# Kernel tuning notes

Hardware: AMD Instinct MI355X
Metric: run time of the kernel (lower is better)

Reference implementation:

```python
import jax, jax.numpy as jnp
import numpy as np

D_MODEL = 2048
NHEADS = 16
HEAD_DIM = D_MODEL // NHEADS


def setup_inputs() -> dict:
    key = jax.random.key(0)
    kx, kq, kk, kv, ko = jax.random.split(key, 5)
    B, S = 2, 2048
    scale = 1.0 / np.sqrt(D_MODEL)
    return {
        "x": jax.random.normal(kx, (B, S, D_MODEL), dtype=jnp.float32),
        "Wq": jax.random.normal(kq, (D_MODEL, D_MODEL), dtype=jnp.float32) * scale,
        "Wk": jax.random.normal(kk, (D_MODEL, D_MODEL), dtype=jnp.float32) * scale,
        "Wv": jax.random.normal(kv, (D_MODEL, D_MODEL), dtype=jnp.float32) * scale,
        "Wo": jax.random.normal(ko, (D_MODEL, D_MODEL), dtype=jnp.float32) * scale,
    }


def reference(x, Wq, Wk, Wv, Wo):
    B, S, _ = x.shape
    # nn.Linear(bias=False): y = x @ W.T
    q = (x @ Wq.T).reshape(B, S, NHEADS, HEAD_DIM)
    k = (x @ Wk.T).reshape(B, S, NHEADS, HEAD_DIM)
    v = (x @ Wv.T).reshape(B, S, NHEADS, HEAD_DIM)
    sm_scale = 1.0 / np.sqrt(HEAD_DIM)
    # scores: [B, H, S, S]
    scores = jnp.einsum("bqhd,bkhd->bhqk", q, k) * sm_scale
    causal_mask = jnp.tril(jnp.ones((S, S), dtype=bool))  # [S, S]
    scores = jnp.where(causal_mask, scores, jnp.finfo(scores.dtype).min)
    probs = jax.nn.softmax(scores, axis=-1)
    attn = jnp.einsum("bhqk,bkhd->bqhd", probs, v)  # [B, S, H, D]
    out = attn.reshape(B, S, D_MODEL) @ Wo.T
    return out
```

## Files before the change

kernel.cpp:

```cpp
#include <hip/hip_runtime.h>
#include <hip/hip_bf16.h>
#include <type_traits>

#define DEV __device__ __forceinline__

typedef __bf16 bf16x8 __attribute__((ext_vector_type(8)));
typedef float f32x4 __attribute__((ext_vector_type(4)));
typedef unsigned short u16;
typedef unsigned int u32;

DEV u16 f32_to_bf16(float f) {
  union { float f; u32 u; } x; x.f = f;
  u32 r = (x.u + 0x7FFFu + ((x.u >> 16) & 1u)) >> 16;
  return (u16)r;
}

DEV void ld_lds16(const void* g, void* l) {
  __builtin_amdgcn_global_load_lds(
      (const __attribute__((address_space(1))) u32*)g,
      (__attribute__((address_space(3))) u32*)l, 16, 0, 0);
}

#define MFMA16(a, b, c) __builtin_amdgcn_mfma_f32_16x16x32_bf16(a, b, c, 0, 0, 0)

__global__ __launch_bounds__(256) void cast_kernel(const float* __restrict__ in,
                                                   u16* __restrict__ out, int n) {
  int i = (blockIdx.x * 256 + threadIdx.x) * 4;
  if (i >= n) return;
  float4 v = *reinterpret_cast<const float4*>(in + i);
  ushort4 o;
  o.x = f32_to_bf16(v.x); o.y = f32_to_bf16(v.y);
  o.z = f32_to_bf16(v.z); o.w = f32_to_bf16(v.w);
  *reinterpret_cast<ushort4*>(out + i) = o;
}

template <typename OutT>
__global__ __launch_bounds__(256) void gemm_nt(const u16* __restrict__ A,
                                               const u16* __restrict__ B,
                                               OutT* __restrict__ C,
                                               int M, int N, int K) {
  __shared__ __align__(16) u16 sA[128 * 64];
  __shared__ __align__(16) u16 sB[128 * 64];
  const int tid = threadIdx.x;
  const int lane = tid & 63, wid = tid >> 6;
  const int lo = lane & 15, hi = lane >> 4;
  const int wm = wid >> 1, wn = wid & 1;
  const int m0 = blockIdx.y * 128, n0 = blockIdx.x * 128;

  f32x4 acc[4][4] = {};

  for (int k0 = 0; k0 < K; k0 += 64) {
    __syncthreads();
#pragma unroll
    for (int i = 0; i < 4; ++i) {
      int e16 = i * 256 + tid;
      int r = e16 >> 3;
      int bcol = ((e16 & 7) * 16) ^ ((r & 7) << 4);
      int col = bcol >> 1;
      ld_lds16(A + (size_t)(m0 + r) * K + k0 + col, sA + e16 * 8);
      ld_lds16(B + (size_t)(n0 + r) * K + k0 + col, sB + e16 * 8);
    }
    __syncthreads();
#pragma unroll
    for (int kc = 0; kc < 2; ++kc) {
      bf16x8 a[4], b[4];
#pragma unroll
      for (int i = 0; i < 4; ++i) {
        int row = wm * 64 + i * 16 + lo;
        int boff = ((kc * 32 + hi * 8) * 2) ^ ((row & 7) << 4);
        a[i] = *(const bf16x8*)((const char*)sA + row * 128 + boff);
      }
#pragma unroll
      for (int i = 0; i < 4; ++i) {
        int row = wn * 64 + i * 16 + lo;
        int boff = ((kc * 32 + hi * 8) * 2) ^ ((row & 7) << 4);
        b[i] = *(const bf16x8*)((const char*)sB + row * 128 + boff);
      }
#pragma unroll
      for (int mi = 0; mi < 4; ++mi)
#pragma unroll
        for (int ni = 0; ni < 4; ++ni)
          acc[mi][ni] = MFMA16(a[mi], b[ni], acc[mi][ni]);
    }
  }
#pragma unroll
  for (int mi = 0; mi < 4; ++mi)
#pragma unroll
    for (int r = 0; r < 4; ++r) {
      size_t row = m0 + wm * 64 + mi * 16 + hi * 4 + r;
#pragma unroll
      for (int ni = 0; ni < 4; ++ni) {
        int col = n0 + wn * 64 + ni * 16 + lo;
        float v = acc[mi][ni][r];
        if constexpr (std::is_same<OutT, float>::value)
          C[row * N + col] = v;
        else
          C[row * N + col] = f32_to_bf16(v);
      }
    }
}

constexpr float SM_SCALE = 0.08838834764831845f;

__global__ __launch_bounds__(256, 2) void attn_fwd(const u16* __restrict__ Q,
                                                   const u16* __restrict__ K,
                                                   const u16* __restrict__ VT,
                                                   u16* __restrict__ O) {
  __shared__ __align__(16) u16 sK[2][64 * 128];
  __shared__ __align__(16) u16 sV[2][128 * 64];
  __shared__ __align__(16) u16 sP[4][16 * 72];

  const int x = blockIdx.x, h = blockIdx.y, b = blockIdx.z;
  const int qt = b ? x : (15 - x);
  const int tid = threadIdx.x;
  const int lane = tid & 63, wid = tid >> 6;
  const int lo = lane & 15, hi = lane >> 4;

  const size_t baseQK = ((size_t)b * 2048) * 2048 + (size_t)h * 128;
  const size_t baseV  = ((size_t)h * 128) * 4096 + (size_t)b * 2048;
  const int q0 = qt * 128;
  const int nt = 2 * qt + 2;

  bf16x8 qf[2][4];
#pragma unroll
  for (int f = 0; f < 2; ++f)
#pragma unroll
    for (int c = 0; c < 4; ++c)
      qf[f][c] = *(const bf16x8*)(Q + baseQK +
                                  (size_t)(q0 + wid * 32 + f * 16 + lo) * 2048 +
                                  c * 32 + hi * 8);

  f32x4 o2[2][8] = {};
  float m[2][4], ls[2][4];
#pragma unroll
  for (int f = 0; f < 2; ++f)
#pragma unroll
    for (int r = 0; r < 4; ++r) { m[f][r] = -INFINITY; ls[f][r] = 0.f; }

  auto stage = [&](int buf, int t) {
    const int kv = t * 64;
#pragma unroll
    for (int i = 0; i < 4; ++i) {
      int e = i * 256 + tid;
      int r = e >> 4;
      int bc = ((e & 15) * 16) ^ ((r & 7) << 4);
      ld_lds16(K + baseQK + (size_t)(kv + r) * 2048 + (bc >> 1), &sK[buf][e * 8]);
    }
#pragma unroll
    for (int i = 0; i < 4; ++i) {
      int e = i * 256 + tid;
      int r = e >> 3;
      int bc = ((e & 7) * 16) ^ ((r & 7) << 4);
      ld_lds16(VT + baseV + (size_t)r * 4096 + kv + (bc >> 1), &sV[buf][e * 8]);
    }
  };

  stage(0, 0);

  for (int t = 0; t < nt; ++t) {
    __syncthreads();
    if (t + 1 < nt) stage((t + 1) & 1, t + 1);
    const u16* bK = sK[t & 1];
    const u16* bV = sV[t & 1];
    const int kv0 = t * 64;

    f32x4 s2[2][4] = {};
#pragma unroll
    for (int n = 0; n < 4; ++n) {
      int row = n * 16 + lo;
#pragma unroll
      for (int c = 0; c < 4; ++c) {
        int boff = ((c * 32 + hi * 8) * 2) ^ ((row & 7) << 4);
        bf16x8 kf = *(const bf16x8*)((const char*)bK + row * 256 + boff);
        s2[0][n] = MFMA16(qf[0][c], kf, s2[0][n]);
        s2[1][n] = MFMA16(qf[1][c], kf, s2[1][n]);
      }
    }

    bf16x8 pf[2][2];
    u16* myP = sP[wid];
#pragma unroll
    for (int f = 0; f < 2; ++f) {
      const int qrow = q0 + wid * 32 + f * 16;
      const bool diag = (kv0 + 63 > qrow);
      float mt[4] = {-3e38f, -3e38f, -3e38f, -3e38f};
#pragma unroll
      for (int n = 0; n < 4; ++n)
#pragma unroll
        for (int r = 0; r < 4; ++r) {
          float xv = s2[f][n][r] * SM_SCALE;
          if (diag && (kv0 + n * 16 + lo > qrow + hi * 4 + r)) xv = -3e38f;
          s2[f][n][r] = xv;
          mt[r] = fmaxf(mt[r], xv);
        }
#pragma unroll
      for (int d = 1; d < 16; d <<= 1)
#pragma unroll
        for (int r = 0; r < 4; ++r) mt[r] = fmaxf(mt[r], __shfl_xor(mt[r], d));

      float fr[4], rs[4];
#pragma unroll
      for (int r = 0; r < 4; ++r) {
        float mn = fmaxf(m[f][r], mt[r]);
        fr[r] = __expf(m[f][r] - mn);
        m[f][r] = mn;
        rs[r] = 0.f;
      }
#pragma unroll
      for (int n = 0; n < 4; ++n)
#pragma unroll
        for (int r = 0; r < 4; ++r) {
          float p = __expf(s2[f][n][r] - m[f][r]);
          s2[f][n][r] = p;
          rs[r] += p;
        }
#pragma unroll
      for (int d = 1; d < 16; d <<= 1)
#pragma unroll
        for (int r = 0; r < 4; ++r) rs[r] += __shfl_xor(rs[r], d);
#pragma unroll
      for (int r = 0; r < 4; ++r) ls[f][r] = ls[f][r] * fr[r] + rs[r];
#pragma unroll
      for (int d8 = 0; d8 < 8; ++d8)
#pragma unroll
        for (int r = 0; r < 4; ++r) o2[f][d8][r] *= fr[r];

#pragma unroll
      for (int n = 0; n < 4; ++n)
#pragma unroll
        for (int r = 0; r < 4; ++r)
          myP[(hi * 4 + r) * 72 + n * 16 + lo] = f32_to_bf16(s2[f][n][r]);
#pragma unroll
      for (int kc = 0; kc < 2; ++kc)
        pf[f][kc] = *(const bf16x8*)(myP + lo * 72 + kc * 32 + hi * 8);
    }

#pragma unroll
    for (int kc = 0; kc < 2; ++kc)
#pragma unroll
      for (int d8 = 0; d8 < 8; ++d8) {
        int row = d8 * 16 + lo;
        int boff = ((kc * 32 + hi * 8) * 2) ^ ((row & 7) << 4);
        bf16x8 vf = *(const bf16x8*)((const char*)bV + row * 128 + boff);
        o2[0][d8] = MFMA16(pf[0][kc], vf, o2[0][d8]);
        o2[1][d8] = MFMA16(pf[1][kc], vf, o2[1][d8]);
      }
  }

#pragma unroll
  for (int f = 0; f < 2; ++f)
#pragma unroll
    for (int r = 0; r < 4; ++r) {
      float inv = 1.f / ls[f][r];
      size_t row = (size_t)b * 2048 + q0 + wid * 32 + f * 16 + hi * 4 + r;
#pragma unroll
      for (int d8 = 0; d8 < 8; ++d8)
        O[row * 2048 + (size_t)h * 128 + d8 * 16 + lo] =
            f32_to_bf16(o2[f][d8][r] * inv);
    }
}

extern "C" void kernel_launch(void* const* d_in, const int* in_sizes, int n_in,
                              void* d_out, int out_size, void* d_ws, size_t ws_size,
                              hipStream_t stream) {
  const float* x  = (const float*)d_in[0];
  const float* Wq = (const float*)d_in[1];
  const float* Wk = (const float*)d_in[2];
  const float* Wv = (const float*)d_in[3];
  const float* Wo = (const float*)d_in[4];
  float* out = (float*)d_out;

  constexpr int B = 2, S = 2048, D = 2048;
  constexpr int M = B * S;

  char* ws = (char*)d_ws;
  u16* xb  = (u16*)ws; ws += (size_t)M * D * 2;
  u16* wqb = (u16*)ws; ws += (size_t)D * D * 2;
  u16* wkb = (u16*)ws; ws += (size_t)D * D * 2;
  u16* wvb = (u16*)ws; ws += (size_t)D * D * 2;
  u16* wob = (u16*)ws; ws += (size_t)D * D * 2;
  u16* q   = (u16*)ws; ws += (size_t)M * D * 2;
  u16* k   = (u16*)ws; ws += (size_t)M * D * 2;
  u16* vT  = (u16*)ws; ws += (size_t)M * D * 2;
  u16* att = (u16*)ws; ws += (size_t)M * D * 2;

  cast_kernel<<<M * D / 1024, 256, 0, stream>>>(x, xb, M * D);
  cast_kernel<<<D * D / 1024, 256, 0, stream>>>(Wq, wqb, D * D);
  cast_kernel<<<D * D / 1024, 256, 0, stream>>>(Wk, wkb, D * D);
  cast_kernel<<<D * D / 1024, 256, 0, stream>>>(Wv, wvb, D * D);
  cast_kernel<<<D * D / 1024, 256, 0, stream>>>(Wo, wob, D * D);

  dim3 gg(D / 128, M / 128);
  gemm_nt<u16><<<gg, 256, 0, stream>>>(xb, wqb, q, M, D, D);
  gemm_nt<u16><<<gg, 256, 0, stream>>>(xb, wkb, k, M, D, D);
  gemm_nt<u16><<<dim3(M / 128, D / 128), 256, 0, stream>>>(wvb, xb, vT, D, M, D);

  attn_fwd<<<dim3(16, 16, B), 256, 0, stream>>>(q, k, vT, att);

  gemm_nt<float><<<gg, 256, 0, stream>>>(att, wob, out, M, D, D);
}
```

Before: 305.7 us.

## Rewrite attention core with 32x32 MFMA, transposed S, register P exchange

Switches the attention inner loop from 16x16x32 to 32x32x16 MFMA and computes S transposed, so each lane owns one query row. Softmax reductions then need only a single cross-half shuffle, and P is repacked into B-operand layout through lane shuffles instead of round-tripping through LDS. It also skips fully masked KV tiles per wave and defers rescaling of the running max unless it grows past a threshold. This trades LDS traffic and wide shuffle reductions for more register pressure and relies on the lazy-rescale bound being numerically safe.

Measured after the change: 278.3 us. -9.0%, faster.

```diff
diff --git a/kernel.cpp b/kernel.cpp
--- a/kernel.cpp
+++ b/kernel.cpp
@@ -6,6 +6,7 @@
 
 typedef __bf16 bf16x8 __attribute__((ext_vector_type(8)));
 typedef float f32x4 __attribute__((ext_vector_type(4)));
+typedef float f32x16 __attribute__((ext_vector_type(16)));
 typedef unsigned short u16;
 typedef unsigned int u32;
 
@@ -15,6 +16,10 @@
   return (u16)r;
 }
 
+DEV u32 pack_bf16(float a, float b) {
+  return (u32)f32_to_bf16(a) | ((u32)f32_to_bf16(b) << 16);
+}
+
 DEV void ld_lds16(const void* g, void* l) {
   __builtin_amdgcn_global_load_lds(
       (const __attribute__((address_space(1))) u32*)g,
@@ -22,6 +27,7 @@
 }
 
 #define MFMA16(a, b, c) __builtin_amdgcn_mfma_f32_16x16x32_bf16(a, b, c, 0, 0, 0)
+#define MFMA32(a, b, c) __builtin_amdgcn_mfma_f32_32x32x16_bf16(a, b, c, 0, 0, 0)
 
 __global__ __launch_bounds__(256) void cast_kernel(const float* __restrict__ in,
                                                    u16* __restrict__ out, int n) {
@@ -101,6 +107,7 @@
 }
 
 constexpr float SM_SCALE = 0.08838834764831845f;
+constexpr float RTHR = 8.0f / SM_SCALE;
 
 __global__ __launch_bounds__(256, 2) void attn_fwd(const u16* __restrict__ Q,
                                                    const u16* __restrict__ K,
@@ -108,34 +115,27 @@
                                                    u16* __restrict__ O) {
   __shared__ __align__(16) u16 sK[2][64 * 128];
   __shared__ __align__(16) u16 sV[2][128 * 64];
-  __shared__ __align__(16) u16 sP[4][16 * 72];
 
   const int x = blockIdx.x, h = blockIdx.y, b = blockIdx.z;
   const int qt = b ? x : (15 - x);
   const int tid = threadIdx.x;
   const int lane = tid & 63, wid = tid >> 6;
-  const int lo = lane & 15, hi = lane >> 4;
+  const int l31 = lane & 31, hi5 = lane >> 5;
 
   const size_t baseQK = ((size_t)b * 2048) * 2048 + (size_t)h * 128;
   const size_t baseV  = ((size_t)h * 128) * 4096 + (size_t)b * 2048;
   const int q0 = qt * 128;
+  const int qw = q0 + wid * 32;
+  const int qg = qw + l31;
   const int nt = 2 * qt + 2;
 
-  bf16x8 qf[2][4];
-#pragma unroll
-  for (int f = 0; f < 2; ++f)
-#pragma unroll
-    for (int c = 0; c < 4; ++c)
-      qf[f][c] = *(const bf16x8*)(Q + baseQK +
-                                  (size_t)(q0 + wid * 32 + f * 16 + lo) * 2048 +
-                                  c * 32 + hi * 8);
-
-  f32x4 o2[2][8] = {};
-  float m[2][4], ls[2][4];
-#pragma unroll
-  for (int f = 0; f < 2; ++f)
-#pragma unroll
-    for (int r = 0; r < 4; ++r) { m[f][r] = -INFINITY; ls[f][r] = 0.f; }
+  bf16x8 qf[8];
+#pragma unroll
+  for (int kc = 0; kc < 8; ++kc)
+    qf[kc] = *(const bf16x8*)(Q + baseQK + (size_t)qg * 2048 + kc * 16 + hi5 * 8);
+
+  f32x16 o[4] = {};
+  float m = -INFINITY, ls = 0.f;
 
   auto stage = [&](int buf, int t) {
     const int kv = t * 64;
@@ -160,103 +160,113 @@
   for (int t = 0; t < nt; ++t) {
     __syncthreads();
     if (t + 1 < nt) stage((t + 1) & 1, t + 1);
+    const int kv0 = t * 64;
+    if (kv0 > qw + 31) continue;
     const u16* bK = sK[t & 1];
     const u16* bV = sV[t & 1];
-    const int kv0 = t * 64;
-
-    f32x4 s2[2][4] = {};
-#pragma unroll
-    for (int n = 0; n < 4; ++n) {
-      int row = n * 16 + lo;
-#pragma unroll
-      for (int c = 0; c < 4; ++c) {
-        int boff = ((c * 32 + hi * 8) * 2) ^ ((row & 7) << 4);
-        bf16x8 kf = *(const bf16x8*)((const char*)bK + row * 256 + boff);
-        s2[0][n] = MFMA16(qf[0][c], kf, s2[0][n]);
-        s2[1][n] = MFMA16(qf[1][c], kf, s2[1][n]);
-      }
-    }
-
-    bf16x8 pf[2][2];
-    u16* myP = sP[wid];
-#pragma unroll
-    for (int f = 0; f < 2; ++f) {
-      const int qrow = q0 + wid * 32 + f * 16;
-      const bool diag = (kv0 + 63 > qrow);
-      float mt[4] = {-3e38f, -3e38f, -3e38f, -3e38f};
-#pragma unroll
-      for (int n = 0; n < 4; ++n)
-#pragma unroll
-        for (int r = 0; r < 4; ++r) {
-          float xv = s2[f][n][r] * SM_SCALE;
-          if (diag && (kv0 + n * 16 + lo > qrow + hi * 4 + r)) xv = -3e38f;
-          s2[f][n][r] = xv;
-          mt[r] = fmaxf(mt[r], xv);
+
+    f32x16 s[2] = {};
+#pragma unroll
+    for (int kb = 0; kb < 2; ++kb) {
+      int row = kb * 32 + l31;
+      int rsw = (row & 7) << 4;
+#pragma unroll
+      for (int kc = 0; kc < 8; ++kc) {
+        int bo = (kc * 32 + hi5 * 16) ^ rsw;
+        bf16x8 kf = *(const bf16x8*)((const char*)bK + row * 256 + bo);
+        s[kb] = MFMA32(kf, qf[kc], s[kb]);
+      }
+    }
+
+    if (kv0 + 63 > qw) {
+#pragma unroll
+      for (int kb = 0; kb < 2; ++kb)
+#pragma unroll
+        for (int j = 0; j < 16; ++j) {
+          int keyg = kv0 + kb * 32 + (j & 3) + 8 * (j >> 2) + 4 * hi5;
+          s[kb][j] = (keyg > qg) ? -3e38f : s[kb][j];
         }
-#pragma unroll
-      for (int d = 1; d < 16; d <<= 1)
-#pragma unroll
-        for (int r = 0; r < 4; ++r) mt[r] = fmaxf(mt[r], __shfl_xor(mt[r], d));
-
-      float fr[4], rs[4];
-#pragma unroll
-      for (int r = 0; r < 4; ++r) {
-        float mn = fmaxf(m[f][r], mt[r]);
-        fr[r] = __expf(m[f][r] - mn);
-        m[f][r] = mn;
-        rs[r] = 0.f;
-      }
-#pragma unroll
-      for (int n = 0; n < 4; ++n)
-#pragma unroll
-        for (int r = 0; r < 4; ++r) {
-          float p = __expf(s2[f][n][r] - m[f][r]);
-          s2[f][n][r] = p;
-          rs[r] += p;
+    }
+
+    float pmax = -3e38f;
+#pragma unroll
+    for (int kb = 0; kb < 2; ++kb)
+#pragma unroll
+      for (int j = 0; j < 16; ++j) pmax = fmaxf(pmax, s[kb][j]);
+    pmax = fmaxf(pmax, __shfl_xor(pmax, 32));
+
+    if (!__all(pmax - m <= RTHR)) {
+      float mn = fmaxf(m, pmax);
+      float fr = __expf((m - mn) * SM_SCALE);
+      ls *= fr;
+#pragma unroll
+      for (int d = 0; d < 4; ++d) o[d] *= fr;
+      m = mn;
+    }
+
+    float rs = 0.f;
+#pragma unroll
+    for (int kb = 0; kb < 2; ++kb)
+#pragma unroll
+      for (int j = 0; j < 16; ++j) {
+        float p = __expf((s[kb][j] - m) * SM_SCALE);
+        s[kb][j] = p;
+        rs += p;
+      }
+    rs += __shfl_xor(rs, 32);
+    ls += rs;
+
+    union PF { u32 w[4]; bf16x8 v; };
+    PF pf[4];
+#pragma unroll
+    for (int kb = 0; kb < 2; ++kb)
+#pragma unroll
+      for (int gp = 0; gp < 2; ++gp) {
+        u32 keep[2], send[2];
+#pragma unroll
+        for (int w = 0; w < 2; ++w) {
+          int ja = 8 * gp + 2 * w;
+          int jb = 8 * gp + 4 + 2 * w;
+          u32 aa = pack_bf16(s[kb][ja], s[kb][ja + 1]);
+          u32 bb = pack_bf16(s[kb][jb], s[kb][jb + 1]);
+          keep[w] = hi5 ? bb : aa;
+          send[w] = hi5 ? aa : bb;
         }
-#pragma unroll
-      for (int d = 1; d < 16; d <<= 1)
-#pragma unroll
-        for (int r = 0; r < 4; ++r) rs[r] += __shfl_xor(rs[r], d);
-#pragma unroll
-      for (int r = 0; r < 4; ++r) ls[f][r] = ls[f][r] * fr[r] + rs[r];
-#pragma unroll
-      for (int d8 = 0; d8 < 8; ++d8)
-#pragma unroll
-        for (int r = 0; r < 4; ++r) o2[f][d8][r] *= fr[r];
-
-#pragma unroll
-      for (int n = 0; n < 4; ++n)
-#pragma unroll
-        for (int r = 0; r < 4; ++r)
-          myP[(hi * 4 + r) * 72 + n * 16 + lo] = f32_to_bf16(s2[f][n][r]);
-#pragma unroll
-      for (int kc = 0; kc < 2; ++kc)
-        pf[f][kc] = *(const bf16x8*)(myP + lo * 72 + kc * 32 + hi * 8);
-    }
-
-#pragma unroll
-    for (int kc = 0; kc < 2; ++kc)
-#pragma unroll
-      for (int d8 = 0; d8 < 8; ++d8) {
-        int row = d8 * 16 + lo;
-        int boff = ((kc * 32 + hi * 8) * 2) ^ ((row & 7) << 4);
-        bf16x8 vf = *(const bf16x8*)((const char*)bV + row * 128 + boff);
-        o2[0][d8] = MFMA16(pf[0][kc], vf, o2[0][d8]);
-        o2[1][d8] = MFMA16(pf[1][kc], vf, o2[1][d8]);
-      }
+        u32 recv0 = (u32)__shfl_xor((int)send[0], 32);
+        u32 recv1 = (u32)__shfl_xor((int)send[1], 32);
+        PF& f = pf[2 * kb + gp];
+        f.w[0] = hi5 ? recv0 : keep[0];
+        f.w[1] = hi5 ? recv1 : keep[1];
+        f.w[2] = hi5 ? keep[0] : recv0;
+        f.w[3] = hi5 ? keep[1] : recv1;
+      }
+
+#pragma unroll
+    for (int d = 0; d < 4; ++d) {
+      int row = d * 32 + l31;
+      int rsw = (row & 7) << 4;
+#pragma unroll
+      for (int ks = 0; ks < 4; ++ks) {
+        int bo = (ks * 32 + hi5 * 16) ^ rsw;
+        bf16x8 vf = *(const bf16x8*)((const char*)bV + row * 128 + bo);
+        o[d] = MFMA32(vf, pf[ks].v, o[d]);
+      }
+    }
   }
 
-#pragma unroll
-  for (int f = 0; f < 2; ++f)
-#pragma unroll
-    for (int r = 0; r < 4; ++r) {
-      float inv = 1.f / ls[f][r];
-      size_t row = (size_t)b * 2048 + q0 + wid * 32 + f * 16 + hi * 4 + r;
-#pragma unroll
-      for (int d8 = 0; d8 < 8; ++d8)
-        O[row * 2048 + (size_t)h * 128 + d8 * 16 + lo] =
-            f32_to_bf16(o2[f][d8][r] * inv);
+  float inv = 1.f / ls;
+  size_t orow = (size_t)b * 2048 + qg;
+#pragma unroll
+  for (int d = 0; d < 4; ++d)
+#pragma unroll
+    for (int G = 0; G < 4; ++G) {
+      ushort4 st;
+      st.x = f32_to_bf16(o[d][4 * G + 0] * inv);
+      st.y = f32_to_bf16(o[d][4 * G + 1] * inv);
+      st.z = f32_to_bf16(o[d][4 * G + 2] * inv);
+      st.w = f32_to_bf16(o[d][4 * G + 3] * inv);
+      int col = h * 128 + d * 32 + 8 * G + 4 * hi5;
+      *(ushort4*)(O + orow * 2048 + col) = st;
     }
 }
 
```
